# Kernel tuning notes

Measured on AMD Instinct MI355X. Metric: run time of the kernel, lower is better.

## Reference

```python
import jax, jax.numpy as jnp
import numpy as np

B, T, C, H, D = 2, 2048, 1024, 16, 64

def setup_inputs() -> dict:
    key = jax.random.key(0)
    ks = jax.random.split(key, 5)
    s = 1.0 / np.sqrt(C)
    return {
        "hidden_states": jax.random.normal(ks[0], (B, T, C), jnp.float32),
        "Wq": jax.random.normal(ks[1], (H, C, D), jnp.float32) * s,
        "Wk": jax.random.normal(ks[2], (H, C, D), jnp.float32) * s,
        "Wv": jax.random.normal(ks[3], (H, C, D), jnp.float32) * s,
        "Wo": jax.random.normal(ks[4], (C, C), jnp.float32) * s,
    }

def reference(hidden_states, Wq, Wk, Wv, Wo):
    x = hidden_states  # (B, T, C)
    q = jnp.einsum("btc,hcd->bhtd", x, Wq)
    k = jnp.einsum("btc,hcd->bhtd", x, Wk)
    v = jnp.einsum("btc,hcd->bhtd", x, Wv)
    scale = 1.0 / jnp.sqrt(jnp.asarray(D, x.dtype))
    scores = jnp.einsum("bhtd,bhsd->bhts", q, k) * scale  # (B,H,T,T)
    Tlen = x.shape[1]
    causal = jnp.tril(jnp.ones((Tlen, Tlen), bool))
    scores = jnp.where(causal, scores, jnp.asarray(-jnp.inf, x.dtype))
    probs = jax.nn.softmax(scores, axis=-1)
    heads = jnp.einsum("bhts,bhsd->bhtd", probs, v)  # (B,H,T,D)
    concat = heads.transpose(0, 2, 1, 3).reshape(x.shape[0], Tlen, H * D)  # (B,T,C)
    return jnp.einsum("btc,oc->bto", concat, Wo)  # output projection (dropout=0)
```

## Files before the change

### kernel.cpp

```cpp
#include <hip/hip_runtime.h>
#include <math.h>

#define B_ 2
#define T_ 2048
#define C_ 1024
#define H_ 16
#define D_ 64

typedef short short8 __attribute__((ext_vector_type(8)));
typedef float f32x4 __attribute__((ext_vector_type(4)));

#define LOG2E 1.44269504088896f

__device__ __forceinline__ unsigned short f2bf(float f) {
    unsigned int u = __float_as_uint(f);
    u += 0x7FFFu + ((u >> 16) & 1u);
    return (unsigned short)(u >> 16);
}
__device__ __forceinline__ unsigned short f2bf_fast(float f) {
    return (unsigned short)((__float_as_uint(f) + 0x8000u) >> 16);
}

__global__ __launch_bounds__(256) void prep_cast(
    const float* __restrict__ x, const float* __restrict__ wo,
    unsigned short* __restrict__ xb, unsigned short* __restrict__ wob,
    int nX, int nW)
{
    int i = (blockIdx.x * 256 + threadIdx.x) * 8;
    const float* s;
    unsigned short* d;
    if (i < nX) { s = x + i; d = xb + i; }
    else {
        int j = i - nX;
        if (j >= nW) return;
        s = wo + j; d = wob + j;
    }
    float4 a = *(const float4*)s;
    float4 b = *(const float4*)(s + 4);
    ushort4 o0, o1;
    o0.x = f2bf(a.x); o0.y = f2bf(a.y); o0.z = f2bf(a.z); o0.w = f2bf(a.w);
    o1.x = f2bf(b.x); o1.y = f2bf(b.y); o1.z = f2bf(b.z); o1.w = f2bf(b.w);
    *(ushort4*)d = o0;
    *(ushort4*)(d + 4) = o1;
}

__global__ __launch_bounds__(256) void transpose_w(
    const float* __restrict__ Wq, const float* __restrict__ Wk,
    const float* __restrict__ Wv,
    unsigned short* __restrict__ Wqt, unsigned short* __restrict__ Wkt,
    unsigned short* __restrict__ Wvt)
{
    __shared__ float t[64][65];
    const int c0 = blockIdx.x * 64;
    const int h  = blockIdx.y;
    const int z  = blockIdx.z;
    const float* W = (z == 0) ? Wq : (z == 1) ? Wk : Wv;
    unsigned short* Wt = (z == 0) ? Wqt : (z == 1) ? Wkt : Wvt;
    const int tid = threadIdx.x;
    const int r = tid >> 4, c4 = (tid & 15) * 4;
    #pragma unroll
    for (int p = 0; p < 4; p++) {
        int cl = r + p * 16;
        float4 v = *(const float4*)&W[((size_t)h * C_ + c0 + cl) * D_ + c4];
        t[cl][c4 + 0] = v.x; t[cl][c4 + 1] = v.y;
        t[cl][c4 + 2] = v.z; t[cl][c4 + 3] = v.w;
    }
    __syncthreads();
    #pragma unroll
    for (int p = 0; p < 4; p++) {
        int d = r + p * 16;
        ushort4 o;
        o.x = f2bf(t[c4 + 0][d]); o.y = f2bf(t[c4 + 1][d]);
        o.z = f2bf(t[c4 + 2][d]); o.w = f2bf(t[c4 + 3][d]);
        *(ushort4*)&Wt[((size_t)h * D_ + d) * C_ + c0 + c4] = o;
    }
}

__global__ __launch_bounds__(256) void qkv_big(
    const unsigned short* __restrict__ X,
    const unsigned short* __restrict__ Wall,
    unsigned short* __restrict__ Qo,
    unsigned short* __restrict__ Ko,
    unsigned short* __restrict__ Vt)
{
    __shared__ unsigned short As[128][72];
    __shared__ unsigned short Bs[128][72];

    const int m0 = blockIdx.x * 128;
    const int n0 = blockIdx.y * 128;
    const int z  = n0 >> 10;
    const int tid = threadIdx.x;
    const int w = tid >> 6, lane = tid & 63, quad = lane >> 4, l16 = lane & 15;
    const int wm = w & 1, wn = w >> 1;
    const int lrow = tid >> 3, lcol = (tid & 7) * 8;

    f32x4 acc[4][4] = {};

    short8 ar[4], br[4];
    #pragma unroll
    for (int p = 0; p < 4; p++) {
        int r = lrow + p * 32;
        ar[p] = *(const short8*)&X[(size_t)(m0 + r) * C_ + lcol];
        br[p] = *(const short8*)&Wall[(size_t)(n0 + r) * C_ + lcol];
    }

    for (int k0 = 0; k0 < C_; k0 += 64) {
        __syncthreads();
        #pragma unroll
        for (int p = 0; p < 4; p++) {
            int r = lrow + p * 32;
            *(short8*)&As[r][lcol] = ar[p];
            *(short8*)&Bs[r][lcol] = br[p];
        }
        __syncthreads();
        if (k0 + 64 < C_) {
            #pragma unroll
            for (int p = 0; p < 4; p++) {
                int r = lrow + p * 32;
                ar[p] = *(const short8*)&X[(size_t)(m0 + r) * C_ + k0 + 64 + lcol];
                br[p] = *(const short8*)&Wall[(size_t)(n0 + r) * C_ + k0 + 64 + lcol];
            }
        }
        #pragma unroll
        for (int ks = 0; ks < 2; ks++) {
            short8 af[4], bf[4];
            #pragma unroll
            for (int i = 0; i < 4; i++)
                af[i] = *(const short8*)&As[wm * 64 + i * 16 + l16][ks * 32 + quad * 8];
            #pragma unroll
            for (int j = 0; j < 4; j++)
                bf[j] = *(const short8*)&Bs[wn * 64 + j * 16 + l16][ks * 32 + quad * 8];
            #pragma unroll
            for (int i = 0; i < 4; i++)
                #pragma unroll
                for (int j = 0; j < 4; j++)
                    acc[i][j] = __builtin_amdgcn_mfma_f32_16x16x32_bf16(af[i], bf[j], acc[i][j], 0, 0, 0);
        }
    }

    if (z == 2) {
        #pragma unroll
        for (int j = 0; j < 4; j++) {
            const int n = n0 + wn * 64 + j * 16 + l16;
            const int h = (n >> 6) & 15, d = n & 63;
            #pragma unroll
            for (int i = 0; i < 4; i++) {
                const int m = m0 + wm * 64 + i * 16 + quad * 4;
                const int b = m >> 11, t = m & (T_ - 1);
                ushort4 pk;
                pk.x = f2bf(acc[i][j][0]);
                pk.y = f2bf(acc[i][j][1]);
                pk.z = f2bf(acc[i][j][2]);
                pk.w = f2bf(acc[i][j][3]);
                *(ushort4*)&Vt[(((size_t)b * H_ + h) * D_ + d) * T_ + t] = pk;
            }
        }
    } else {
        const float scale = (z == 0) ? 0.125f * LOG2E : 1.0f;
        unsigned short* O = (z == 0) ? Qo : Ko;
        #pragma unroll
        for (int j = 0; j < 4; j++) {
            const int n = n0 + wn * 64 + j * 16 + l16;
            const int h = (n >> 6) & 15, d = n & 63;
            #pragma unroll
            for (int i = 0; i < 4; i++)
                #pragma unroll
                for (int r = 0; r < 4; r++) {
                    const int m = m0 + wm * 64 + i * 16 + quad * 4 + r;
                    const int b = m >> 11, t = m & (T_ - 1);
                    O[(((size_t)b * H_ + h) * T_ + t) * D_ + d] = f2bf(acc[i][j][r] * scale);
                }
        }
    }
}

__global__ __launch_bounds__(512, 4) void flash_mfma(
    const unsigned short* __restrict__ Q,
    const unsigned short* __restrict__ K,
    const unsigned short* __restrict__ Vt,
    unsigned short* __restrict__ CC)
{
    __shared__ unsigned short kst[2][64][72];
    __shared__ unsigned short vts[2][64][72];
    __shared__ unsigned short ps [2][64][72];

    const int pairid = blockIdx.x, h = blockIdx.y, b = blockIdx.z;
    const int tid = threadIdx.x;
    const int g  = tid >> 8;
    const int t2 = tid & 255;
    const int w = t2 >> 6, lane = t2 & 63, quad = lane >> 4, l16 = lane & 15;
    const int lrow = t2 >> 3, lcol = (t2 & 7) * 8;
    const size_t hb  = ((size_t)b * H_ + h) * T_;
    const size_t hbD = ((size_t)b * H_ + h) * D_;

    float* fob = (float*)&kst[0][0][0];
    float* flb = (float*)&ps[0][0][0];

    for (int phase = 0; phase < 2; phase++) {
        const int qb = phase ? 31 - pairid : pairid;
        const int q0 = qb * 64;
        const int nkb = qb + 1;
        const int maxit = (nkb + 1) >> 1;

        short8 qf[2];
        #pragma unroll
        for (int ks = 0; ks < 2; ks++)
            qf[ks] = *(const short8*)&Q[(hb + q0 + w * 16 + l16) * D_ + ks * 32 + quad * 8];

        float l_part[4] = {0.f, 0.f, 0.f, 0.f};
        f32x4 o[4] = {};

        short8 kreg[2], vreg[2];
        {
            const int k0 = g * 64;
            #pragma unroll
            for (int p = 0; p < 2; p++) {
                int r = lrow + p * 32;
                kreg[p] = *(const short8*)&K[(hb + k0 + r) * D_ + lcol];
                vreg[p] = *(const short8*)&Vt[(hbD + r) * T_ + k0 + lcol];
            }
        }

        for (int it = 0; it < maxit; it++) {
            const int kb = 2 * it + g;
            const bool act = (kb < nkb);
            __syncthreads();
            if (act) {
                #pragma unroll
                for (int p = 0; p < 2; p++) {
                    int r = lrow + p * 32;
                    *(short8*)&kst[g][r][lcol] = kreg[p];
                    *(short8*)&vts[g][r][lcol] = vreg[p];
                }
            }
            __syncthreads();
            if (kb + 2 < nkb) {
                const int k0n = (kb + 2) * 64;
                #pragma unroll
                for (int p = 0; p < 2; p++) {
                    int r = lrow + p * 32;
                    kreg[p] = *(const short8*)&K[(hb + k0n + r) * D_ + lcol];
                    vreg[p] = *(const short8*)&Vt[(hbD + r) * T_ + k0n + lcol];
                }
            }
            if (act) {
                f32x4 s[4] = {};
                #pragma unroll
                for (int ks = 0; ks < 2; ks++)
                    #pragma unroll
                    for (int ct = 0; ct < 4; ct++) {
                        short8 kf = *(const short8*)&kst[g][ct * 16 + l16][ks * 32 + quad * 8];
                        s[ct] = __builtin_amdgcn_mfma_f32_16x16x32_bf16(qf[ks], kf, s[ct], 0, 0, 0);
                    }

                if (kb == qb) {
                    #pragma unroll
                    for (int ct = 0; ct < 4; ct++)
                        #pragma unroll
                        for (int r = 0; r < 4; r++) {
                            int qr = w * 16 + quad * 4 + r;
                            int kc = ct * 16 + l16;
                            if (kc > qr) s[ct][r] = -INFINITY;
                        }
                }

                #pragma unroll
                for (int ct = 0; ct < 4; ct++)
                    #pragma unroll
                    for (int r = 0; r < 4; r++) {
                        float p = exp2f(s[ct][r]);
                        l_part[r] += p;
                        ps[g][w * 16 + quad * 4 + r][ct * 16 + l16] = f2bf_fast(p);
                    }

                #pragma unroll
                for (int ks = 0; ks < 2; ks++) {
                    short8 pa = *(const short8*)&ps[g][w * 16 + l16][ks * 32 + quad * 8];
                    #pragma unroll
                    for (int ct = 0; ct < 4; ct++) {
                        short8 vf = *(const short8*)&vts[g][ct * 16 + l16][ks * 32 + quad * 8];
                        o[ct] = __builtin_amdgcn_mfma_f32_16x16x32_bf16(pa, vf, o[ct], 0, 0, 0);
                    }
                }
            }
        }

        __syncthreads();
        if (g == 1) {
            #pragma unroll
            for (int r = 0; r < 4; r++) {
                float ls = l_part[r];
                ls += __shfl_xor(ls, 1);
                ls += __shfl_xor(ls, 2);
                ls += __shfl_xor(ls, 4);
                ls += __shfl_xor(ls, 8);
                if (l16 == 0) flb[w * 16 + quad * 4 + r] = ls;
                #pragma unroll
                for (int ct = 0; ct < 4; ct++)
                    fob[(w * 16 + quad * 4 + r) * 68 + ct * 16 + l16] = o[ct][r];
            }
        }
        __syncthreads();
        if (g == 0) {
            #pragma unroll
            for (int r = 0; r < 4; r++) {
                float ls = l_part[r];
                ls += __shfl_xor(ls, 1);
                ls += __shfl_xor(ls, 2);
                ls += __shfl_xor(ls, 4);
                ls += __shfl_xor(ls, 8);
                const int q = w * 16 + quad * 4 + r;
                ls += flb[q];
                const float invl = 1.0f / ls;
                const int t = q0 + q;
                #pragma unroll
                for (int ct = 0; ct < 4; ct++) {
                    float ov = o[ct][r] + fob[q * 68 + ct * 16 + l16];
                    CC[((size_t)b * T_ + t) * C_ + h * D_ + ct * 16 + l16] = f2bf(ov * invl);
                }
            }
        }
        __syncthreads();
    }
}

__global__ __launch_bounds__(256) void out_big(
    const unsigned short* __restrict__ X,
    const unsigned short* __restrict__ Wob,
    float* __restrict__ out)
{
    __shared__ unsigned short As[128][72];
    __shared__ unsigned short Bs[128][72];

    const int m0 = blockIdx.x * 128;
    const int n0 = blockIdx.y * 128;
    const int tid = threadIdx.x;
    const int w = tid >> 6, lane = tid & 63, quad = lane >> 4, l16 = lane & 15;
    const int wm = w & 1, wn = w >> 1;
    const int lrow = tid >> 3, lcol = (tid & 7) * 8;

    f32x4 acc[4][4] = {};

    short8 ar[4], br[4];
    #pragma unroll
    for (int p = 0; p < 4; p++) {
        int r = lrow + p * 32;
        ar[p] = *(const short8*)&X[(size_t)(m0 + r) * C_ + lcol];
        br[p] = *(const short8*)&Wob[(size_t)(n0 + r) * C_ + lcol];
    }

    for (int k0 = 0; k0 < C_; k0 += 64) {
        __syncthreads();
        #pragma unroll
        for (int p = 0; p < 4; p++) {
            int r = lrow + p * 32;
            *(short8*)&As[r][lcol] = ar[p];
            *(short8*)&Bs[r][lcol] = br[p];
        }
        __syncthreads();
        if (k0 + 64 < C_) {
            #pragma unroll
            for (int p = 0; p < 4; p++) {
                int r = lrow + p * 32;
                ar[p] = *(const short8*)&X[(size_t)(m0 + r) * C_ + k0 + 64 + lcol];
                br[p] = *(const short8*)&Wob[(size_t)(n0 + r) * C_ + k0 + 64 + lcol];
            }
        }
        #pragma unroll
        for (int ks = 0; ks < 2; ks++) {
            short8 af[4], bf[4];
            #pragma unroll
            for (int i = 0; i < 4; i++)
                af[i] = *(const short8*)&As[wm * 64 + i * 16 + l16][ks * 32 + quad * 8];
            #pragma unroll
            for (int j = 0; j < 4; j++)
                bf[j] = *(const short8*)&Bs[wn * 64 + j * 16 + l16][ks * 32 + quad * 8];
            #pragma unroll
            for (int i = 0; i < 4; i++)
                #pragma unroll
                for (int j = 0; j < 4; j++)
                    acc[i][j] = __builtin_amdgcn_mfma_f32_16x16x32_bf16(af[i], bf[j], acc[i][j], 0, 0, 0);
        }
    }

    #pragma unroll
    for (int i = 0; i < 4; i++)
        #pragma unroll
        for (int j = 0; j < 4; j++)
            #pragma unroll
            for (int r = 0; r < 4; r++)
                out[(size_t)(m0 + wm * 64 + i * 16 + quad * 4 + r) * C_ + n0 + wn * 64 + j * 16 + l16] = acc[i][j][r];
}

extern "C" void kernel_launch(void* const* d_in, const int* in_sizes, int n_in,
                              void* d_out, int out_size, void* d_ws, size_t ws_size,
                              hipStream_t stream) {
    const float* x  = (const float*)d_in[0];
    const float* Wq = (const float*)d_in[1];
    const float* Wk = (const float*)d_in[2];
    const float* Wv = (const float*)d_in[3];
    const float* Wo = (const float*)d_in[4];
    float* out = (float*)d_out;

    const size_t nX = (size_t)B_ * T_ * C_;
    const size_t nW = (size_t)H_ * C_ * D_;
    const size_t nQ = (size_t)B_ * H_ * T_ * D_;
    unsigned short* xb   = (unsigned short*)d_ws;
    unsigned short* Wall = xb + nX;
    unsigned short* Wqt  = Wall;
    unsigned short* Wkt  = Wqt + nW;
    unsigned short* Wvt  = Wkt + nW;
    unsigned short* Wob  = Wvt + nW;
    unsigned short* Qb   = Wob + nW;
    unsigned short* Kb   = Qb + nQ;
    unsigned short* Vtb  = Kb + nQ;
    unsigned short* CCb  = Vtb + nQ;

    prep_cast<<<dim3((unsigned)((nX + nW) / 2048)), 256, 0, stream>>>(
        x, Wo, xb, Wob, (int)nX, (int)nW);
    transpose_w<<<dim3(C_ / 64, H_, 3), 256, 0, stream>>>(Wq, Wk, Wv, Wqt, Wkt, Wvt);
    qkv_big<<<dim3(32, 24), 256, 0, stream>>>(xb, Wall, Qb, Kb, Vtb);
    flash_mfma<<<dim3(16, H_, B_), 512, 0, stream>>>(Qb, Kb, Vtb, CCb);
    out_big<<<dim3(32, 8), 256, 0, stream>>>(CCb, Wob, out);
}
```

Measured before the change: 181.8 us.

## Merge prep kernels and use direct global-to-LDS loads with XOR swizzle in QKV GEMM

Fuses the bf16 cast and weight-transpose kernels into one launch, removing a kernel launch boundary. The QKV GEMM now loads tiles straight from global memory into LDS using global_load_lds, with an XOR-swizzled unpadded layout to avoid bank conflicts, instead of staging them through registers. This drops the register prefetch, so global loads are no longer overlapped with MFMA compute within a block. Occupancy and other resident blocks have to hide that latency instead.

```diff
diff --git a/kernel.cpp b/kernel.cpp
--- a/kernel.cpp
+++ b/kernel.cpp
@@ -21,42 +21,49 @@
     return (unsigned short)((__float_as_uint(f) + 0x8000u) >> 16);
 }
 
-__global__ __launch_bounds__(256) void prep_cast(
-    const float* __restrict__ x, const float* __restrict__ wo,
-    unsigned short* __restrict__ xb, unsigned short* __restrict__ wob,
-    int nX, int nW)
+__device__ __forceinline__ void gld16(const unsigned short* g, unsigned short* l) {
+    __builtin_amdgcn_global_load_lds(
+        (const __attribute__((address_space(1))) void*)g,
+        (__attribute__((address_space(3))) void*)l, 16, 0, 0);
+}
+
+#define NCAST 2560
+
+__global__ __launch_bounds__(256) void prep_all(
+    const float* __restrict__ x,  const float* __restrict__ Wq,
+    const float* __restrict__ Wk, const float* __restrict__ Wv,
+    const float* __restrict__ Wo,
+    unsigned short* __restrict__ xb,   unsigned short* __restrict__ Wall,
+    unsigned short* __restrict__ wob,  int nX, int nW)
 {
-    int i = (blockIdx.x * 256 + threadIdx.x) * 8;
-    const float* s;
-    unsigned short* d;
-    if (i < nX) { s = x + i; d = xb + i; }
-    else {
-        int j = i - nX;
-        if (j >= nW) return;
-        s = wo + j; d = wob + j;
-    }
-    float4 a = *(const float4*)s;
-    float4 b = *(const float4*)(s + 4);
-    ushort4 o0, o1;
-    o0.x = f2bf(a.x); o0.y = f2bf(a.y); o0.z = f2bf(a.z); o0.w = f2bf(a.w);
-    o1.x = f2bf(b.x); o1.y = f2bf(b.y); o1.z = f2bf(b.z); o1.w = f2bf(b.w);
-    *(ushort4*)d = o0;
-    *(ushort4*)(d + 4) = o1;
-}
-
-__global__ __launch_bounds__(256) void transpose_w(
-    const float* __restrict__ Wq, const float* __restrict__ Wk,
-    const float* __restrict__ Wv,
-    unsigned short* __restrict__ Wqt, unsigned short* __restrict__ Wkt,
-    unsigned short* __restrict__ Wvt)
-{
+    const int bid = blockIdx.x;
+    const int tid = threadIdx.x;
+    if (bid < NCAST) {
+        int i = (bid * 256 + tid) * 8;
+        const float* s;
+        unsigned short* d;
+        if (i < nX) { s = x + i; d = xb + i; }
+        else {
+            int j = i - nX;
+            if (j >= nW) return;
+            s = Wo + j; d = wob + j;
+        }
+        float4 a = *(const float4*)s;
+        float4 b = *(const float4*)(s + 4);
+        ushort4 o0, o1;
+        o0.x = f2bf(a.x); o0.y = f2bf(a.y); o0.z = f2bf(a.z); o0.w = f2bf(a.w);
+        o1.x = f2bf(b.x); o1.y = f2bf(b.y); o1.z = f2bf(b.z); o1.w = f2bf(b.w);
+        *(ushort4*)d = o0;
+        *(ushort4*)(d + 4) = o1;
+        return;
+    }
     __shared__ float t[64][65];
-    const int c0 = blockIdx.x * 64;
-    const int h  = blockIdx.y;
-    const int z  = blockIdx.z;
+    const int tb = bid - NCAST;
+    const int c0 = (tb & 15) * 64;
+    const int h  = (tb >> 4) & 15;
+    const int z  = tb >> 8;
     const float* W = (z == 0) ? Wq : (z == 1) ? Wk : Wv;
-    unsigned short* Wt = (z == 0) ? Wqt : (z == 1) ? Wkt : Wvt;
-    const int tid = threadIdx.x;
+    unsigned short* Wt = Wall + (size_t)z * H_ * D_ * C_;
     const int r = tid >> 4, c4 = (tid & 15) * 4;
     #pragma unroll
     for (int p = 0; p < 4; p++) {
@@ -83,8 +90,8 @@
     unsigned short* __restrict__ Ko,
     unsigned short* __restrict__ Vt)
 {
-    __shared__ unsigned short As[128][72];
-    __shared__ unsigned short Bs[128][72];
+    __shared__ __align__(16) unsigned short As[128 * 64];
+    __shared__ __align__(16) unsigned short Bs[128 * 64];
 
     const int m0 = blockIdx.x * 128;
     const int n0 = blockIdx.y * 128;
@@ -92,44 +99,32 @@
     const int tid = threadIdx.x;
     const int w = tid >> 6, lane = tid & 63, quad = lane >> 4, l16 = lane & 15;
     const int wm = w & 1, wn = w >> 1;
-    const int lrow = tid >> 3, lcol = (tid & 7) * 8;
+    const int lr8 = lane >> 3, gc = (lane & 7) ^ lr8;
 
     f32x4 acc[4][4] = {};
 
-    short8 ar[4], br[4];
-    #pragma unroll
-    for (int p = 0; p < 4; p++) {
-        int r = lrow + p * 32;
-        ar[p] = *(const short8*)&X[(size_t)(m0 + r) * C_ + lcol];
-        br[p] = *(const short8*)&Wall[(size_t)(n0 + r) * C_ + lcol];
-    }
-
     for (int k0 = 0; k0 < C_; k0 += 64) {
         __syncthreads();
         #pragma unroll
         for (int p = 0; p < 4; p++) {
-            int r = lrow + p * 32;
-            *(short8*)&As[r][lcol] = ar[p];
-            *(short8*)&Bs[r][lcol] = br[p];
-        }
-        __syncthreads();
-        if (k0 + 64 < C_) {
-            #pragma unroll
-            for (int p = 0; p < 4; p++) {
-                int r = lrow + p * 32;
-                ar[p] = *(const short8*)&X[(size_t)(m0 + r) * C_ + k0 + 64 + lcol];
-                br[p] = *(const short8*)&Wall[(size_t)(n0 + r) * C_ + k0 + 64 + lcol];
-            }
-        }
+            const int row = w * 32 + p * 8;
+            gld16(&X[(size_t)(m0 + row + lr8) * C_ + k0 + gc * 8],    &As[row * 64]);
+            gld16(&Wall[(size_t)(n0 + row + lr8) * C_ + k0 + gc * 8], &Bs[row * 64]);
+        }
+        __syncthreads();
         #pragma unroll
         for (int ks = 0; ks < 2; ks++) {
             short8 af[4], bf[4];
             #pragma unroll
-            for (int i = 0; i < 4; i++)
-                af[i] = *(const short8*)&As[wm * 64 + i * 16 + l16][ks * 32 + quad * 8];
-            #pragma unroll
-            for (int j = 0; j < 4; j++)
-                bf[j] = *(const short8*)&Bs[wn * 64 + j * 16 + l16][ks * 32 + quad * 8];
+            for (int i = 0; i < 4; i++) {
+                const int r = wm * 64 + i * 16 + l16;
+                af[i] = *(const short8*)&As[r * 64 + (((ks * 4 + quad) ^ (l16 & 7)) * 8)];
+            }
+            #pragma unroll
+            for (int j = 0; j < 4; j++) {
+                const int r = wn * 64 + j * 16 + l16;
+                bf[j] = *(const short8*)&Bs[r * 64 + (((ks * 4 + quad) ^ (l16 & 7)) * 8)];
+            }
             #pragma unroll
             for (int i = 0; i < 4; i++)
                 #pragma unroll
@@ -407,18 +402,14 @@
     const size_t nQ = (size_t)B_ * H_ * T_ * D_;
     unsigned short* xb   = (unsigned short*)d_ws;
     unsigned short* Wall = xb + nX;
-    unsigned short* Wqt  = Wall;
-    unsigned short* Wkt  = Wqt + nW;
-    unsigned short* Wvt  = Wkt + nW;
-    unsigned short* Wob  = Wvt + nW;
+    unsigned short* Wob  = Wall + 3 * nW;
     unsigned short* Qb   = Wob + nW;
     unsigned short* Kb   = Qb + nQ;
     unsigned short* Vtb  = Kb + nQ;
     unsigned short* CCb  = Vtb + nQ;
 
-    prep_cast<<<dim3((unsigned)((nX + nW) / 2048)), 256, 0, stream>>>(
-        x, Wo, xb, Wob, (int)nX, (int)nW);
-    transpose_w<<<dim3(C_ / 64, H_, 3), 256, 0, stream>>>(Wq, Wk, Wv, Wqt, Wkt, Wvt);
+    prep_all<<<dim3(NCAST + 768), 256, 0, stream>>>(
+        x, Wq, Wk, Wv, Wo, xb, Wall, Wob, (int)nX, (int)nW);
     qkv_big<<<dim3(32, 24), 256, 0, stream>>>(xb, Wall, Qb, Kb, Vtb);
     flash_mfma<<<dim3(16, H_, B_), 512, 0, stream>>>(Qb, Kb, Vtb, CCb);
     out_big<<<dim3(32, 8), 256, 0, stream>>>(CCb, Wob, out);
```

Result: slower. 187.4 us (+3.1%).
